# Optimization experiments

Measured on AMD Instinct MI355X. Metric: run time of the kernel, lower is better.

## Reference

```python
import jax, jax.numpy as jnp
import numpy as np

HIDDEN = 2048
N_HEADS = 16
HEAD_DIM = HIDDEN // N_HEADS
ROPE_BASE = 10000.0


def rotate_half(x):
    half = x.shape[-1] // 2
    return jnp.concatenate((-x[..., half:], x[..., :half]), axis=-1)


def rope_cos_sin(seq_len, dtype):
    inv_freq = 1.0 / (ROPE_BASE ** (jnp.arange(0, HEAD_DIM, 2, dtype=jnp.float32) / HEAD_DIM))
    pos = jnp.arange(seq_len, dtype=jnp.float32)
    freqs = jnp.einsum('i,j->ij', pos, inv_freq)  # [S, hd/2]
    emb = jnp.concatenate((freqs, freqs), axis=-1)  # [S, hd]
    return jnp.cos(emb).astype(dtype), jnp.sin(emb).astype(dtype)


def setup_inputs() -> dict:
    key = jax.random.key(0)
    ks = jax.random.split(key, 9)
    B, S, H = 2, 2048, HIDDEN
    std = 1.0 / np.sqrt(H)
    return {
        'hidden_states': jax.random.normal(ks[0], (B, S, H), dtype=jnp.float32),
        'Wq': jax.random.uniform(ks[1], (H, H), jnp.float32, -std, std),
        'bq': jax.random.uniform(ks[2], (H,), jnp.float32, -std, std),
        'Wk': jax.random.uniform(ks[3], (H, H), jnp.float32, -std, std),
        'bk': jax.random.uniform(ks[4], (H,), jnp.float32, -std, std),
        'Wv': jax.random.uniform(ks[5], (H, H), jnp.float32, -std, std),
        'bv': jax.random.uniform(ks[6], (H,), jnp.float32, -std, std),
        'Wo': jax.random.uniform(ks[7], (H, H), jnp.float32, -std, std),
        'bo': jax.random.uniform(ks[8], (H,), jnp.float32, -std, std),
    }


def reference(hidden_states, Wq, bq, Wk, bk, Wv, bv, Wo, bo):
    B, S, H = hidden_states.shape
    scale = HEAD_DIM ** -0.5

    def proj(W, b):
        # torch Linear: x @ W.T + b
        y = jnp.einsum('bsh,oh->bso', hidden_states, W) + b
        return y.reshape(B, S, N_HEADS, HEAD_DIM).transpose(0, 2, 1, 3)  # [B,nh,S,hd]

    q = proj(Wq, bq)
    k = proj(Wk, bk)
    v = proj(Wv, bv)

    cos, sin = rope_cos_sin(S, hidden_states.dtype)  # [S, hd]
    cos = cos[None, None, :, :]
    sin = sin[None, None, :, :]
    q = q * cos + rotate_half(q) * sin
    k = k * cos + rotate_half(k) * sin

    scores = jnp.einsum('bhqd,bhkd->bhqk', q, k) * scale  # [B,nh,S,S]
    probs = jax.nn.softmax(scores, axis=-1)
    ctx = jnp.einsum('bhqk,bhkd->bhqd', probs, v)
    ctx = ctx.transpose(0, 2, 1, 3).reshape(B, S, H)
    return jnp.einsum('bsh,oh->bso', ctx, Wo) + bo
```

## Files before the change

### kernel.cpp

```cpp
#include <hip/hip_runtime.h>
#include <hip/hip_bf16.h>
#include <math.h>

#define HIDDEN 2048
#define NH 16
#define HD 128
#define NB 2
#define SEQ 2048
#define K_DIM 2048

typedef unsigned int u32;
typedef unsigned short ushort_t;
typedef __bf16 bf16x8 __attribute__((ext_vector_type(8)));
typedef float f32x4 __attribute__((ext_vector_type(4)));
typedef ushort_t u16x8 __attribute__((ext_vector_type(8)));

__device__ __forceinline__ void split1(float x, unsigned short& h, unsigned short& l) {
    u32 u = __float_as_uint(x);
    u32 hr = (u + 0x7FFFu + ((u >> 16) & 1u)) >> 16;
    h = (unsigned short)hr;
    float r = x - __uint_as_float(hr << 16);
    u32 u2 = __float_as_uint(r);
    l = (unsigned short)((u2 + 0x7FFFu + ((u2 >> 16) & 1u)) >> 16);
}

__device__ __forceinline__ ushort_t bf16r(float x) {
    u32 u = __float_as_uint(x);
    return (ushort_t)((u + 0x7FFFu + ((u >> 16) & 1u)) >> 16);
}

__device__ __forceinline__ void gl_lds16(const void* g, void* l) {
    __builtin_amdgcn_global_load_lds(
        (const __attribute__((address_space(1))) u32*)g,
        (__attribute__((address_space(3))) u32*)l, 16, 0, 0);
}

__global__ void k_rope_tables(float* __restrict__ ct, float* __restrict__ st) {
    int idx = blockIdx.x * 256 + threadIdx.x;
    int s = idx >> 6, d = idx & 63;
    double inv = pow(10000.0, -(double)d * (1.0 / 64.0));
    double ang = (double)s * inv;
    ct[idx] = (float)cos(ang);
    st[idx] = (float)sin(ang);
}

#define XG 2097152
#define WG 1048576
__global__ void k_cvt_all(const float4* __restrict__ X, const float4* __restrict__ W0,
                          const float4* __restrict__ W1, const float4* __restrict__ W2,
                          ushort4* __restrict__ Xh, ushort4* __restrict__ H0,
                          ushort4* __restrict__ H1, ushort4* __restrict__ H2) {
    int idx = blockIdx.x * 256 + threadIdx.x;
    const float4* src;
    ushort4* dst;
    int off;
    if (idx < XG) { src = X; dst = Xh; off = idx; }
    else {
        int t = idx - XG;
        int m = t >> 20;
        off = t & (WG - 1);
        src = (m == 0) ? W0 : (m == 1) ? W1 : W2;
        dst = (m == 0) ? H0 : (m == 1) ? H1 : H2;
    }
    float4 x = src[off];
    ushort4 h;
    h.x = bf16r(x.x); h.y = bf16r(x.y); h.z = bf16r(x.z); h.w = bf16r(x.w);
    dst[off] = h;
}

__global__ void k_split(const float4* __restrict__ src, ushort4* __restrict__ hi,
                        ushort4* __restrict__ lo) {
    int idx = blockIdx.x * 256 + threadIdx.x;
    float4 x = src[idx];
    ushort4 h, l;
    split1(x.x, h.x, l.x);
    split1(x.y, h.y, l.y);
    split1(x.z, h.z, l.z);
    split1(x.w, h.w, l.w);
    hi[idx] = h;
    lo[idx] = l;
}

#define BAR  __builtin_amdgcn_s_barrier()
#define LGKM0 asm volatile("s_waitcnt lgkmcnt(0)" ::: "memory")
#define VM4  asm volatile("s_waitcnt vmcnt(4)" ::: "memory")
#define VM0  asm volatile("s_waitcnt vmcnt(0)" ::: "memory")
#define PRIO1 __builtin_amdgcn_s_setprio(1)
#define PRIO0 __builtin_amdgcn_s_setprio(0)

#define STA(slot, half, kt) do { \
    const ushort_t* g_ = Xh + sgA + (size_t)((half) * 128) * 2048 + (size_t)(kt) * 64; \
    gl_lds16(g_, &As[slot][((half) * 128 + w * 16) * 64]); \
    gl_lds16(g_ + 8 * 2048, &As[slot][((half) * 128 + w * 16 + 8) * 64]); \
} while (0)

#define STB(slot, half, kt) do { \
    const ushort_t* g_ = Wsel + sgB + (size_t)((half) * 128) * 2048 + (size_t)(kt) * 64; \
    gl_lds16(g_, &Bs[slot][((half) * 128 + w * 16) * 64]); \
    gl_lds16(g_ + 8 * 2048, &Bs[slot][((half) * 128 + w * 16 + 8) * 64]); \
} while (0)

#define RD_A4(DST, slot, MB) \
    _Pragma("unroll") for (int mf = 0; mf < 4; mf++) { \
        DST[mf][0] = *(const bf16x8*)&As[slot][arow + ((MB) + mf) * 1024 + cc0]; \
        DST[mf][1] = *(const bf16x8*)&As[slot][arow + ((MB) + mf) * 1024 + cc1]; \
    }

#define RD_B2(DST, slot, NBB) \
    _Pragma("unroll") for (int nf = 0; nf < 2; nf++) { \
        DST[nf][0] = *(const bf16x8*)&Bs[slot][brow + ((NBB) + nf) * 1024 + cc0]; \
        DST[nf][1] = *(const bf16x8*)&Bs[slot][brow + ((NBB) + nf) * 1024 + cc1]; \
    }

#define PH_MFMA(AF, BF, MB, NBB) do { PRIO1; \
    _Pragma("unroll") for (int mf = 0; mf < 4; mf++) \
    _Pragma("unroll") for (int nf = 0; nf < 2; nf++) { \
        acc[(MB) + mf][(NBB) + nf] = __builtin_amdgcn_mfma_f32_16x16x32_bf16( \
            AF[mf][0], BF[nf][0], acc[(MB) + mf][(NBB) + nf], 0, 0, 0); \
        acc[(MB) + mf][(NBB) + nf] = __builtin_amdgcn_mfma_f32_16x16x32_bf16( \
            AF[mf][1], BF[nf][1], acc[(MB) + mf][(NBB) + nf], 0, 0, 0); \
    } PRIO0; } while (0)

__global__ __launch_bounds__(512, 2)
void k_gemm_qkv8(const ushort_t* __restrict__ Xh,
                 const ushort_t* __restrict__ W0, const ushort_t* __restrict__ W1,
                 const ushort_t* __restrict__ W2,
                 const float* __restrict__ b0, const float* __restrict__ b1,
                 const float* __restrict__ b2,
                 float* __restrict__ o0, float* __restrict__ o1, float* __restrict__ o2) {
    __shared__ ushort_t As[2][256 * 64];
    __shared__ ushort_t Bs[2][256 * 64];
    const int tid = threadIdx.x;
    const int lane = tid & 63;
    const int w = tid >> 6;
    const int wm = w >> 2;
    const int wn = w & 3;
    const int quad = lane >> 4;
    const int l15 = lane & 15;

    int bid = blockIdx.x;
    bid = (bid & 7) * 48 + (bid >> 3);
    const int bx = bid & 15;
    const int by = bid >> 4;
    const int m0 = bx << 8;
    const int mat = by >> 3;
    const int n0 = (by & 7) << 8;
    const ushort_t* Wsel = (mat == 0) ? W0 : (mat == 1) ? W1 : W2;
    const float* bias = (mat == 0) ? b0 : (mat == 1) ? b1 : b2;
    float* out = (mat == 0) ? o0 : (mat == 1) ? o1 : o2;

    const int lrow = lane >> 3;
    const int lcol8 = (((lane & 7) ^ lrow) << 3);
    const size_t sgA = (size_t)(m0 + w * 16 + lrow) * 2048 + lcol8;
    const size_t sgB = (size_t)(n0 + w * 16 + lrow) * 2048 + lcol8;

    const int arow = (wm * 128 + l15) * 64;
    const int brow = (wn * 64 + l15) * 64;
    const int cc0 = ((quad ^ (l15 & 7)) << 3);
    const int cc1 = cc0 ^ 32;

    f32x4 acc[8][4];
#pragma unroll
    for (int i = 0; i < 8; i++)
#pragma unroll
        for (int j = 0; j < 4; j++) acc[i][j] = (f32x4){0.f, 0.f, 0.f, 0.f};

    STA(0, 0, 0); STA(0, 1, 0);
    STB(0, 0, 0); STB(0, 1, 0);
    STA(1, 0, 1); STA(1, 1, 1);

    bf16x8 a03[4][2], a47[4][2], b01[2][2], b23[2][2];

    for (int it = 0; it < 16; ++it) {
        const int kt0 = 2 * it, kt1 = 2 * it + 1;
        const bool st = (it < 15);
        VM4; BAR;
        RD_A4(a03, 0, 0); RD_B2(b01, 0, 0);
        STB(1, 0, kt1);
        BAR; LGKM0;
        PH_MFMA(a03, b01, 0, 0);
        BAR;
        RD_A4(a47, 0, 4); RD_B2(b23, 0, 2);
        STB(1, 1, kt1);
        BAR; LGKM0;
        PH_MFMA(a03, b23, 0, 2);
        BAR;
        if (st) STA(0, 0, kt0 + 2);
        BAR;
        PH_MFMA(a47, b01, 4, 0);
        BAR;
        if (st) STA(0, 1, kt0 + 2);
        BAR;
        PH_MFMA(a47, b23, 4, 2);
        if (it == 15) { VM0; } else { VM4; }
        BAR;
        RD_A4(a03, 1, 0); RD_B2(b01, 1, 0);
        if (st) STB(0, 0, kt0 + 2);
        BAR; LGKM0;
        PH_MFMA(a03, b01, 0, 0);
        BAR;
        RD_A4(a47, 1, 4); RD_B2(b23, 1, 2);
        if (st) STB(0, 1, kt0 + 2);
        BAR; LGKM0;
        PH_MFMA(a03, b23, 0, 2);
        BAR;
        if (st) STA(1, 0, kt1 + 2);
        BAR;
        PH_MFMA(a47, b01, 4, 0);
        BAR;
        if (st) STA(1, 1, kt1 + 2);
        BAR;
        PH_MFMA(a47, b23, 4, 2);
    }

    float bcolv[4];
#pragma unroll
    for (int nf = 0; nf < 4; nf++) bcolv[nf] = bias[n0 + wn * 64 + nf * 16 + l15];

    const int mbase = m0 + wm * 128 + quad * 4;
#pragma unroll
    for (int mf = 0; mf < 8; mf++)
#pragma unroll
        for (int nf = 0; nf < 4; nf++) {
            const int n = n0 + wn * 64 + nf * 16 + l15;
            const int hh = n >> 7;
            const int d = n & 127;
#pragma unroll
            for (int r = 0; r < 4; r++) {
                const int m = mbase + mf * 16 + r;
                const int bb = m >> 11;
                const int s = m & (SEQ - 1);
                out[((size_t)(bb * NH + hh) * SEQ + s) * HD + d] = acc[mf][nf][r] + bcolv[nf];
            }
        }
}

__global__ __launch_bounds__(256)
void k_gemm_o(const ushort_t* __restrict__ Ah, const ushort_t* __restrict__ Al,
              const ushort_t* __restrict__ Bh, const ushort_t* __restrict__ Bl,
              const float* __restrict__ bias, float* __restrict__ out) {
    __shared__ ushort_t lds[4][128 * 32];
    const int tid = threadIdx.x;
    const int lane = tid & 63;
    const int w = tid >> 6;
    const int wm = w & 1, wn = w >> 1;
    const int quad = lane >> 4;
    const int l15 = lane & 15;
    const int m0 = blockIdx.x << 7;
    const int n0 = blockIdx.y << 7;
    const bool isA = (w < 2);

    const ushort_t* src = (w == 0) ? Ah : (w == 1) ? Al : (w == 2) ? Bh : Bl;
    const int lrow = lane >> 2;
    const int lk = (lane & 3) << 3;
    const ushort_t* gp[8];
    ushort_t* lp[8];
#pragma unroll
    for (int i = 0; i < 8; i++) {
        if (isA) {
            int m = m0 + i * 16 + lrow;
            int bb = m >> 11, s = m & (SEQ - 1);
            gp[i] = src + ((size_t)bb * NH * SEQ + s) * HD + lk;
        } else {
            gp[i] = src + (size_t)(n0 + i * 16 + lrow) * K_DIM + lk;
        }
        lp[i] = &lds[w][i * 512];
    }

    f32x4 acc[4][4];
#pragma unroll
    for (int i = 0; i < 4; i++)
#pragma unroll
        for (int j = 0; j < 4; j++) acc[i][j] = (f32x4){0.f, 0.f, 0.f, 0.f};

    const int aoff = (wm * 64 + l15) * 32 + quad * 8;
    const int boff = (wn * 64 + l15) * 32 + quad * 8;

#pragma unroll
    for (int i = 0; i < 8; i++) gl_lds16(gp[i], lp[i]);
    __syncthreads();
    bf16x8 ah[4], al[4], bh[4], bl[4];
#pragma unroll
    for (int f = 0; f < 4; f++) {
        ah[f] = *(const bf16x8*)&lds[0][aoff + f * 512];
        al[f] = *(const bf16x8*)&lds[1][aoff + f * 512];
        bh[f] = *(const bf16x8*)&lds[2][boff + f * 512];
        bl[f] = *(const bf16x8*)&lds[3][boff + f * 512];
    }

    for (int kt = 32; kt <= K_DIM; kt += 32) {
        __syncthreads();
        if (kt < K_DIM) {
            const size_t koff = isA ? ((size_t)(kt >> 7) * (SEQ * HD) + (kt & 127)) : (size_t)kt;
#pragma unroll
            for (int i = 0; i < 8; i++) gl_lds16(gp[i] + koff, lp[i]);
        }
#pragma unroll
        for (int fm = 0; fm < 4; fm++)
#pragma unroll
            for (int fn = 0; fn < 4; fn++) {
                acc[fm][fn] = __builtin_amdgcn_mfma_f32_16x16x32_bf16(ah[fm], bh[fn], acc[fm][fn], 0, 0, 0);
                acc[fm][fn] = __builtin_amdgcn_mfma_f32_16x16x32_bf16(ah[fm], bl[fn], acc[fm][fn], 0, 0, 0);
                acc[fm][fn] = __builtin_amdgcn_mfma_f32_16x16x32_bf16(al[fm], bh[fn], acc[fm][fn], 0, 0, 0);
            }
        if (kt < K_DIM) {
            __syncthreads();
#pragma unroll
            for (int f = 0; f < 4; f++) {
                ah[f] = *(const bf16x8*)&lds[0][aoff + f * 512];
                al[f] = *(const bf16x8*)&lds[1][aoff + f * 512];
                bh[f] = *(const bf16x8*)&lds[2][boff + f * 512];
                bl[f] = *(const bf16x8*)&lds[3][boff + f * 512];
            }
        }
    }

    float bcolv[4];
#pragma unroll
    for (int fn = 0; fn < 4; fn++) bcolv[fn] = bias[n0 + wn * 64 + fn * 16 + l15];

    const int mb = m0 + wm * 64 + quad * 4;
    const int nb = n0 + wn * 64 + l15;
#pragma unroll
    for (int fm = 0; fm < 4; fm++)
#pragma unroll
        for (int fn = 0; fn < 4; fn++)
#pragma unroll
            for (int r = 0; r < 4; r++)
                out[(size_t)(mb + fm * 16 + r) * HIDDEN + nb + fn * 16] =
                    acc[fm][fn][r] + bcolv[fn];
}

__global__ void k_rope_pack(const float* __restrict__ q, const float* __restrict__ k,
                            const float* __restrict__ ct, const float* __restrict__ st,
                            ushort_t* __restrict__ Qb, ushort_t* __restrict__ Kb) {
    int idx = blockIdx.x * 256 + threadIdx.x;
    int d = idx & 63;
    int s = (idx >> 6) & (SEQ - 1);
    int bh = idx >> 17;
    size_t base = ((size_t)bh * SEQ + s) * HD;
    float c = ct[(s << 6) + d], sn = st[(s << 6) + d];
    const float scq = 0.08838834764831845f;
    float q0 = q[base + d], q1 = q[base + d + 64];
    Qb[base + d]      = bf16r((q0 * c - q1 * sn) * scq);
    Qb[base + d + 64] = bf16r((q1 * c + q0 * sn) * scq);
    float k0 = k[base + d], k1 = k[base + d + 64];
    Kb[base + d]      = bf16r(k0 * c - k1 * sn);
    Kb[base + d + 64] = bf16r(k1 * c + k0 * sn);
}

__global__ __launch_bounds__(256)
void k_vpack(const float* __restrict__ v, ushort_t* __restrict__ vt) {
    __shared__ float t[64][65];
    const int tid = threadIdx.x;
    const int bh = blockIdx.z;
    const int s0 = blockIdx.x << 6;
    const int d0 = blockIdx.y << 6;
    const float* src = v + ((size_t)bh * SEQ + s0) * HD + d0;
    const int rr = tid >> 4;
    const int cc = (tid & 15) << 2;
#pragma unroll
    for (int i = 0; i < 4; i++) {
        float4 x = *(const float4*)(src + (size_t)(i * 16 + rr) * HD + cc);
        t[i * 16 + rr][cc] = x.x;
        t[i * 16 + rr][cc + 1] = x.y;
        t[i * 16 + rr][cc + 2] = x.z;
        t[i * 16 + rr][cc + 3] = x.w;
    }
    __syncthreads();
    const int dr = tid >> 2;
    const int sc_ = (tid & 3) << 4;
    ushort_t* dst = vt + ((size_t)bh * HD + d0 + dr) * SEQ + s0 + sc_;
    u16x8 o0, o1;
#pragma unroll
    for (int u = 0; u < 8; u++) o0[u] = bf16r(t[sc_ + u][dr]);
#pragma unroll
    for (int u = 0; u < 8; u++) o1[u] = bf16r(t[sc_ + 8 + u][dr]);
    *(u16x8*)dst = o0;
    *(u16x8*)(dst + 8) = o1;
}

__global__ __launch_bounds__(256, 2)
void k_flash_mfma(const ushort_t* __restrict__ Qb, const ushort_t* __restrict__ Kb,
                  const ushort_t* __restrict__ Vt,
                  ushort_t* __restrict__ ch, ushort_t* __restrict__ cl) {
    __shared__ ushort_t KV[128 * 136];
    __shared__ ushort_t Ps[128 * 136];
    const int tid = threadIdx.x;
    const int lane = tid & 63;
    const int w = tid >> 6;
    const int quad = lane >> 4;
    const int l15 = lane & 15;
    const int bi = blockIdx.x;
    const int bh = bi & 31;
    const int qt = bi >> 5;
    const ushort_t* Qg = Qb + ((size_t)bh * SEQ + ((size_t)qt << 7)) * HD;
    const ushort_t* Kg = Kb + (size_t)bh * SEQ * HD;
    const ushort_t* Vg = Vt + (size_t)bh * HD * SEQ;

    bf16x8 qf[2][4];
#pragma unroll
    for (int qi = 0; qi < 2; qi++)
#pragma unroll
        for (int ks = 0; ks < 4; ks++)
            qf[qi][ks] = *(const bf16x8*)(Qg + (size_t)(w * 32 + qi * 16 + l15) * HD + ks * 32 + quad * 8);

    const int sr = tid >> 4;
    const int sc8 = (tid & 15) << 3;

    u16x8 Kreg[8], Vreg[8];
#pragma unroll
    for (int i = 0; i < 8; i++)
        Kreg[i] = *(const u16x8*)(Kg + (size_t)(i * 16 + sr) * HD + sc8);
#pragma unroll
    for (int i = 0; i < 8; i++)
        Vreg[i] = *(const u16x8*)(Vg + (size_t)(i * 16 + sr) * SEQ + sc8);

    f32x4 acc[2][8];
#pragma unroll
    for (int qi = 0; qi < 2; qi++)
#pragma unroll
        for (int d = 0; d < 8; d++) acc[qi][d] = (f32x4){0.f, 0.f, 0.f, 0.f};
    float lp[2] = {0.f, 0.f};

    for (int kt = 0; kt < SEQ; kt += 128) {
        const int np = kt + 128;
        __syncthreads();
#pragma unroll
        for (int i = 0; i < 8; i++)
            *(u16x8*)&KV[(i * 16 + sr) * 136 + sc8] = Kreg[i];
        if (np < SEQ) {
#pragma unroll
            for (int i = 0; i < 8; i++)
                Kreg[i] = *(const u16x8*)(Kg + (size_t)(np + i * 16 + sr) * HD + sc8);
        }
        __syncthreads();

        f32x4 sc[2][8];
#pragma unroll
        for (int qi = 0; qi < 2; qi++)
#pragma unroll
            for (int j = 0; j < 8; j++) sc[qi][j] = (f32x4){0.f, 0.f, 0.f, 0.f};
#pragma unroll
        for (int ks = 0; ks < 4; ks++) {
#pragma unroll
            for (int jh = 0; jh < 2; jh++) {
                bf16x8 kf[4];
#pragma unroll
                for (int j = 0; j < 4; j++)
                    kf[j] = *(const bf16x8*)&KV[((jh * 4 + j) * 16 + l15) * 136 + ks * 32 + quad * 8];
#pragma unroll
                for (int qi = 0; qi < 2; qi++)
#pragma unroll
                    for (int j = 0; j < 4; j++)
                        sc[qi][jh * 4 + j] = __builtin_amdgcn_mfma_f32_16x16x32_bf16(
                            kf[j], qf[qi][ks], sc[qi][jh * 4 + j], 0, 0, 0);
            }
        }

#pragma unroll
        for (int qi = 0; qi < 2; qi++) {
            const int prow = (w * 32 + qi * 16 + l15) * 136 + quad * 4;
#pragma unroll
            for (int j = 0; j < 8; j++) {
                float p0 = __expf(sc[qi][j][0]);
                float p1 = __expf(sc[qi][j][1]);
                float p2 = __expf(sc[qi][j][2]);
                float p3 = __expf(sc[qi][j][3]);
                lp[qi] += (p0 + p1) + (p2 + p3);
                __hip_bfloat162 lo2 = __float22bfloat162_rn({p0, p1});
                __hip_bfloat162 hi2 = __float22bfloat162_rn({p2, p3});
                uint2 pk = make_uint2(*(u32*)&lo2, *(u32*)&hi2);
                *(uint2*)&Ps[prow + j * 16] = pk;
            }
        }
        __syncthreads();
#pragma unroll
        for (int i = 0; i < 8; i++)
            *(u16x8*)&KV[(i * 16 + sr) * 136 + sc8] = Vreg[i];
        if (np < SEQ) {
#pragma unroll
            for (int i = 0; i < 8; i++)
                Vreg[i] = *(const u16x8*)(Vg + (size_t)(i * 16 + sr) * SEQ + np + sc8);
        }
        __syncthreads();

#pragma unroll
        for (int ks = 0; ks < 4; ks++) {
            bf16x8 pf[2];
#pragma unroll
            for (int qi = 0; qi < 2; qi++)
                pf[qi] = *(const bf16x8*)&Ps[(w * 32 + qi * 16 + l15) * 136 + ks * 32 + quad * 8];
#pragma unroll
            for (int db = 0; db < 8; db++) {
                bf16x8 vf = *(const bf16x8*)&KV[(db * 16 + l15) * 136 + ks * 32 + quad * 8];
#pragma unroll
                for (int qi = 0; qi < 2; qi++)
                    acc[qi][db] = __builtin_amdgcn_mfma_f32_16x16x32_bf16(vf, pf[qi], acc[qi][db], 0, 0, 0);
            }
        }
    }

    float inv[2];
#pragma unroll
    for (int qi = 0; qi < 2; qi++) {
        float l = lp[qi];
        l += __shfl_xor(l, 16);
        l += __shfl_xor(l, 32);
        inv[qi] = 1.0f / l;
    }
    const size_t obase = ((size_t)bh * SEQ + ((size_t)qt << 7)) * HD;

    __syncthreads();
#pragma unroll
    for (int qi = 0; qi < 2; qi++)
#pragma unroll
        for (int db = 0; db < 8; db++) {
            ushort4 hh;
            ushort_t dum;
            split1(acc[qi][db][0] * inv[qi], hh.x, dum);
            split1(acc[qi][db][1] * inv[qi], hh.y, dum);
            split1(acc[qi][db][2] * inv[qi], hh.z, dum);
            split1(acc[qi][db][3] * inv[qi], hh.w, dum);
            *(ushort4*)&Ps[(w * 32 + qi * 16 + l15) * 136 + db * 16 + quad * 4] = hh;
        }
    __syncthreads();
#pragma unroll
    for (int t = 0; t < 8; t++) {
        int c = t * 256 + tid;
        int row = c >> 4, col8 = (c & 15) << 3;
        *(u16x8*)&ch[obase + (size_t)row * HD + col8] = *(const u16x8*)&Ps[row * 136 + col8];
    }
    __syncthreads();
#pragma unroll
    for (int qi = 0; qi < 2; qi++)
#pragma unroll
        for (int db = 0; db < 8; db++) {
            ushort4 ll;
            ushort_t dum;
            split1(acc[qi][db][0] * inv[qi], dum, ll.x);
            split1(acc[qi][db][1] * inv[qi], dum, ll.y);
            split1(acc[qi][db][2] * inv[qi], dum, ll.z);
            split1(acc[qi][db][3] * inv[qi], dum, ll.w);
            *(ushort4*)&Ps[(w * 32 + qi * 16 + l15) * 136 + db * 16 + quad * 4] = ll;
        }
    __syncthreads();
#pragma unroll
    for (int t = 0; t < 8; t++) {
        int c = t * 256 + tid;
        int row = c >> 4, col8 = (c & 15) << 3;
        *(u16x8*)&cl[obase + (size_t)row * HD + col8] = *(const u16x8*)&Ps[row * 136 + col8];
    }
}

extern "C" void kernel_launch(void* const* d_in, const int* in_sizes, int n_in,
                              void* d_out, int out_size, void* d_ws, size_t ws_size,
                              hipStream_t stream) {
    const float* X  = (const float*)d_in[0];
    const float* Wq = (const float*)d_in[1];
    const float* bq = (const float*)d_in[2];
    const float* Wk = (const float*)d_in[3];
    const float* bk = (const float*)d_in[4];
    const float* Wv = (const float*)d_in[5];
    const float* bv = (const float*)d_in[6];
    const float* Wo = (const float*)d_in[7];
    const float* bo = (const float*)d_in[8];
    float* out = (float*)d_out;

    const size_t QS = (size_t)NB * NH * SEQ * HD;
    const size_t WS = (size_t)HIDDEN * HIDDEN;
    float* q_ws = (float*)d_ws;
    float* k_ws = q_ws + QS;
    float* v_ws = k_ws + QS;
    float* cost = v_ws + QS;
    float* sint = cost + (size_t)SEQ * 64;
    ushort_t* Xh = (ushort_t*)(sint + (size_t)SEQ * 64);
    ushort_t* Wh0 = Xh + QS;
    ushort_t* Wh1 = Wh0 + WS;
    ushort_t* Wh2 = Wh1 + WS;
    ushort_t* Woh = Wh2 + WS;
    ushort_t* Wol = Woh + WS;
    ushort_t* Kb  = Wol + WS;
    ushort_t* Vtb = Kb + QS;
    ushort_t* ctxh = (ushort_t*)q_ws;
    ushort_t* ctxl = ctxh + QS;

    k_rope_tables<<<(SEQ * 64) / 256, 256, 0, stream>>>(cost, sint);

    k_cvt_all<<<(XG + 3 * WG) / 256, 256, 0, stream>>>(
        (const float4*)X, (const float4*)Wq, (const float4*)Wk, (const float4*)Wv,
        (ushort4*)Xh, (ushort4*)Wh0, (ushort4*)Wh1, (ushort4*)Wh2);
    k_split<<<WS / 4 / 256, 256, 0, stream>>>((const float4*)Wo, (ushort4*)Woh, (ushort4*)Wol);

    k_gemm_qkv8<<<384, 512, 0, stream>>>(Xh, Wh0, Wh1, Wh2, bq, bk, bv,
                                         q_ws, k_ws, v_ws);

    ushort_t* Qbb = Xh;
    k_rope_pack<<<(NB * NH * SEQ * 64) / 256, 256, 0, stream>>>(q_ws, k_ws, cost, sint, Qbb, Kb);
    k_vpack<<<dim3(SEQ / 64, HD / 64, NB * NH), 256, 0, stream>>>(v_ws, Vtb);

    k_flash_mfma<<<512, 256, 0, stream>>>(Qbb, Kb, Vtb, ctxh, ctxl);

    k_gemm_o<<<dim3(32, 16), 256, 0, stream>>>(ctxh, ctxl, Woh, Wol, bo, out);
}
```

Baseline: 504.4 us.

## Simplify QKV GEMM main loop to coarse double-buffered k-tile pipeline

Replaces the fine-grained 8-phase interleaved schedule, with many barriers and partial LDS stages, by a coarse double-buffer. Each step stages a whole k-tile into the other slot, waits with vmcnt(8), then reads all fragments and issues all MFMAs for the current slot. This cuts the barrier count and explicit lgkmcnt waits. In exchange it loses the fine overlap of LDS reads with MFMA and holds more fragment registers live at once.

```diff
diff --git a/kernel.cpp b/kernel.cpp
--- a/kernel.cpp
+++ b/kernel.cpp
@@ -82,8 +82,7 @@
 }
 
 #define BAR  __builtin_amdgcn_s_barrier()
-#define LGKM0 asm volatile("s_waitcnt lgkmcnt(0)" ::: "memory")
-#define VM4  asm volatile("s_waitcnt vmcnt(4)" ::: "memory")
+#define VM8  asm volatile("s_waitcnt vmcnt(8)" ::: "memory")
 #define VM0  asm volatile("s_waitcnt vmcnt(0)" ::: "memory")
 #define PRIO1 __builtin_amdgcn_s_setprio(1)
 #define PRIO0 __builtin_amdgcn_s_setprio(0)
@@ -98,6 +97,10 @@
     const ushort_t* g_ = Wsel + sgB + (size_t)((half) * 128) * 2048 + (size_t)(kt) * 64; \
     gl_lds16(g_, &Bs[slot][((half) * 128 + w * 16) * 64]); \
     gl_lds16(g_ + 8 * 2048, &Bs[slot][((half) * 128 + w * 16 + 8) * 64]); \
+} while (0)
+
+#define STAGE_T(slot, kt) do { \
+    STA(slot, 0, kt); STA(slot, 1, kt); STB(slot, 0, kt); STB(slot, 1, kt); \
 } while (0)
 
 #define RD_A4(DST, slot, MB) \
@@ -120,6 +123,15 @@
         acc[(MB) + mf][(NBB) + nf] = __builtin_amdgcn_mfma_f32_16x16x32_bf16( \
             AF[mf][1], BF[nf][1], acc[(MB) + mf][(NBB) + nf], 0, 0, 0); \
     } PRIO0; } while (0)
+
+#define KTILE(slot) do { \
+    RD_A4(a03, slot, 0); RD_B2(b01, slot, 0); \
+    RD_A4(a47, slot, 4); RD_B2(b23, slot, 2); \
+    PH_MFMA(a03, b01, 0, 0); \
+    PH_MFMA(a47, b01, 4, 0); \
+    PH_MFMA(a03, b23, 0, 2); \
+    PH_MFMA(a47, b23, 4, 2); \
+} while (0)
 
 __global__ __launch_bounds__(512, 2)
 void k_gemm_qkv8(const ushort_t* __restrict__ Xh,
@@ -165,52 +177,20 @@
 #pragma unroll
         for (int j = 0; j < 4; j++) acc[i][j] = (f32x4){0.f, 0.f, 0.f, 0.f};
 
-    STA(0, 0, 0); STA(0, 1, 0);
-    STB(0, 0, 0); STB(0, 1, 0);
-    STA(1, 0, 1); STA(1, 1, 1);
-
     bf16x8 a03[4][2], a47[4][2], b01[2][2], b23[2][2];
 
+    STAGE_T(0, 0);
+
     for (int it = 0; it < 16; ++it) {
-        const int kt0 = 2 * it, kt1 = 2 * it + 1;
-        const bool st = (it < 15);
-        VM4; BAR;
-        RD_A4(a03, 0, 0); RD_B2(b01, 0, 0);
-        STB(1, 0, kt1);
-        BAR; LGKM0;
-        PH_MFMA(a03, b01, 0, 0);
+        STAGE_T(1, 2 * it + 1);
+        VM8;
         BAR;
-        RD_A4(a47, 0, 4); RD_B2(b23, 0, 2);
-        STB(1, 1, kt1);
-        BAR; LGKM0;
-        PH_MFMA(a03, b23, 0, 2);
+        KTILE(0);
         BAR;
-        if (st) STA(0, 0, kt0 + 2);
+        if (it < 15) { STAGE_T(0, 2 * it + 2); VM8; } else { VM0; }
         BAR;
-        PH_MFMA(a47, b01, 4, 0);
+        KTILE(1);
         BAR;
-        if (st) STA(0, 1, kt0 + 2);
-        BAR;
-        PH_MFMA(a47, b23, 4, 2);
-        if (it == 15) { VM0; } else { VM4; }
-        BAR;
-        RD_A4(a03, 1, 0); RD_B2(b01, 1, 0);
-        if (st) STB(0, 0, kt0 + 2);
-        BAR; LGKM0;
-        PH_MFMA(a03, b01, 0, 0);
-        BAR;
-        RD_A4(a47, 1, 4); RD_B2(b23, 1, 2);
-        if (st) STB(0, 1, kt0 + 2);
-        BAR; LGKM0;
-        PH_MFMA(a03, b23, 0, 2);
-        BAR;
-        if (st) STA(1, 0, kt1 + 2);
-        BAR;
-        PH_MFMA(a47, b01, 4, 0);
-        BAR;
-        if (st) STA(1, 1, kt1 + 2);
-        BAR;
-        PH_MFMA(a47, b23, 4, 2);
     }
 
     float bcolv[4];
```

Measured after the change: 495.4 us. About the same (-1.8%).
